# Performance work log

Hardware: AMD Instinct MI355X
Metric: run time of the kernel (lower is better)

The kernel has to match this reference:

```python
import jax, jax.numpy as jnp
import numpy as np

N, IN, C, H, NC, E, G = 4096, 16, 128, 2, 4, 131072, 64
EPS = 1e-5


def setup_inputs() -> dict:
    key = jax.random.key(0)
    ks = jax.random.split(key, 12)
    def rn(k, shape, scale=0.05):
        return jax.random.normal(k, shape, dtype=jnp.float32) * scale
    return dict(
        x=rn(ks[0], (N, IN), 1.0),
        edge_index=jax.random.randint(ks[1], (2, E), 0, N, dtype=jnp.int32),
        batch=jnp.sort(jax.random.randint(ks[2], (N,), 0, G, dtype=jnp.int32)),
        proj_W=rn(ks[3], (IN, C)), proj_b=jnp.zeros((C,), jnp.float32),
        gcn_W=rn(ks[4], (2, C, C)), gcn_b=jnp.zeros((2, C), jnp.float32),
        attn_qkv_w=rn(ks[5], (2, 3 * C, C)), attn_qkv_b=jnp.zeros((2, 3 * C), jnp.float32),
        attn_out_w=rn(ks[6], (2, C, C)), attn_out_b=jnp.zeros((2, C), jnp.float32),
        bn_gamma=jnp.ones((2, 3, C), jnp.float32), bn_beta=jnp.zeros((2, 3, C), jnp.float32),
        mlp_W1=rn(ks[7], (2, C, 2 * C)), mlp_b1=jnp.zeros((2, 2 * C), jnp.float32),
        mlp_W2=rn(ks[8], (2, 2 * C, C)), mlp_b2=jnp.zeros((2, C), jnp.float32),
        lin_W=rn(ks[9], (C, NC)), lin_b=jnp.zeros((NC,), jnp.float32),
    )


def _bn(h, g, b):
    # PyG BatchNorm (training-mode stats over the node dim, biased var)
    mu = jnp.mean(h, axis=0)
    var = jnp.mean((h - mu) ** 2, axis=0)
    return (h - mu) * jax.lax.rsqrt(var + EPS) * g + b


def _gcn(h_in, W, b, src, dst):
    # GCNConv: x' = D^-1/2 (A+I) D^-1/2 (x W) + b
    h = h_in @ W
    deg = jnp.zeros((N,), h.dtype).at[dst].add(1.0) + 1.0  # +1 self loop
    dinv = jax.lax.rsqrt(deg)
    coef = dinv[src] * dinv[dst]                           # [E]
    out = jax.ops.segment_sum(h[src] * coef[:, None], dst, num_segments=N)
    out = out + h * (dinv * dinv)[:, None]                 # self-loop term
    return out + b


def _mha(x, wqkv, bqkv, wout, bout):
    # batch=None in the source => attention over all N nodes as one sequence
    qkv = x @ wqkv.T + bqkv                                # [N,3C]
    q, k, v = jnp.split(qkv, 3, axis=-1)
    dh = C // H
    q = q.reshape(N, H, dh) * (dh ** -0.5)
    k = k.reshape(N, H, dh)
    v = v.reshape(N, H, dh)
    a = jax.nn.softmax(jnp.einsum('nhd,mhd->hnm', q, k), axis=-1)  # [H,N,N]
    o = jnp.einsum('hnm,mhd->nhd', a, v).reshape(N, C)
    return o @ wout.T + bout


def _forward(x, proj_W, proj_b, gcn_W, gcn_b, attn_qkv_w, attn_qkv_b,
             attn_out_w, attn_out_b, bn_gamma, bn_beta, mlp_W1, mlp_b1,
             mlp_W2, mlp_b2, lin_W, lin_b, edge_index, batch):
    src, dst = edge_index[0], edge_index[1]
    h = x @ proj_W + proj_b
    for l in range(2):  # two structurally-distinct GPS layers
        hl = _bn(_gcn(h, gcn_W[l], gcn_b[l], src, dst) + h, bn_gamma[l, 0], bn_beta[l, 0])
        ha = _bn(_mha(h, attn_qkv_w[l], attn_qkv_b[l], attn_out_w[l], attn_out_b[l]) + h,
                 bn_gamma[l, 1], bn_beta[l, 1])
        o = hl + ha
        m = jax.nn.relu(o @ mlp_W1[l] + mlp_b1[l]) @ mlp_W2[l] + mlp_b2[l]
        h = _bn(o + m, bn_gamma[l, 2], bn_beta[l, 2])
        if l == 0:
            h = jax.nn.relu(h)
    ssum = jax.ops.segment_sum(h, batch, num_segments=G)
    cnt = jax.ops.segment_sum(jnp.ones((N,), h.dtype), batch, num_segments=G)
    pooled = ssum / jnp.maximum(cnt, 1.0)[:, None]
    return pooled @ lin_W + lin_b


def reference(x, edge_index, batch, proj_W, proj_b, gcn_W, gcn_b,
              attn_qkv_w, attn_qkv_b, attn_out_w, attn_out_b,
              bn_gamma, bn_beta, mlp_W1, mlp_b1, mlp_W2, mlp_b2,
              lin_W, lin_b):
    return _forward(x, proj_W, proj_b, gcn_W, gcn_b, attn_qkv_w, attn_qkv_b,
                    attn_out_w, attn_out_b, bn_gamma, bn_beta, mlp_W1, mlp_b1,
                    mlp_W2, mlp_b2, lin_W, lin_b, edge_index, batch)
```

## Files before the change

### kernel.cpp

```cpp
#include <hip/hip_runtime.h>
#include <hip/hip_bf16.h>


constexpr int N_  = 4096;
constexpr int IN_ = 16;
constexpr int C_  = 128;
constexpr int E_  = 131072;
constexpr int G_  = 64;
constexpr float EPSV = 1e-5f;
constexpr int SP_ = 8;

typedef unsigned short u16;
typedef unsigned int u32;
typedef __attribute__((ext_vector_type(8))) short bf16x8;
typedef __attribute__((ext_vector_type(4))) short bf16x4;
typedef __attribute__((ext_vector_type(8))) unsigned short u16x8;
typedef __attribute__((ext_vector_type(4))) float f32x4;

__device__ inline u16 f2bf(float f) {
  union { __hip_bfloat16 b; u16 u; } v;
  v.b = __float2bfloat16(f);
  return v.u;
}
__device__ inline float bf2f(u16 s) {
  union { unsigned u; float f; } v; v.u = ((unsigned)s) << 16;
  return v.f;
}

__global__ __launch_bounds__(256) void prol_k(const float* __restrict__ x,
                                              const float* __restrict__ projW,
                                              const float* __restrict__ projB,
                                              float* __restrict__ h,
                                              const float* __restrict__ gcnW,
                                              const float* __restrict__ qkvW,
                                              const float* __restrict__ outW,
                                              const float* __restrict__ w1,
                                              const float* __restrict__ w2,
                                              u16* __restrict__ Wh,
                                              u16* __restrict__ Wl,
                                              const int* __restrict__ ei,
                                              int* __restrict__ cnt) {
  const int bx = blockIdx.x;
  const int tid = threadIdx.x;
  if (bx < 2048) {
    int idx = bx * 256 + tid;
    int n = idx >> 7, c = idx & 127;
    float acc = projB[c];
#pragma unroll
    for (int k = 0; k < IN_; ++k) acc = fmaf(x[n * IN_ + k], projW[k * C_ + c], acc);
    h[idx] = acc;
    return;
  }
  if (bx >= 2336) {
    int e = (bx - 2336) * 256 + tid;
    atomicAdd(&cnt[ei[E_ + e]], 1);
    return;
  }
  int wb = bx - 2048;
  int l = wb / 144, b = wb % 144;
  const float* src; int dstOff, K, M, trans;
  if (b < 16)       { src = gcnW + l * 16384; dstOff = 0;      K = 128; M = 128; trans = 0; }
  else if (b < 64)  { src = qkvW + l * 49152; dstOff = 16384;  K = 128; M = 0;   trans = 1; b -= 16; }
  else if (b < 80)  { src = outW + l * 16384; dstOff = 65536;  K = 128; M = 0;   trans = 1; b -= 64; }
  else if (b < 112) { src = w1 + l * 32768;   dstOff = 81920;  K = 128; M = 256; trans = 0; b -= 80; }
  else              { src = w2 + l * 32768;   dstOff = 114688; K = 256; M = 128; trans = 0; b -= 112; }
  dstOff += l * 147456;
  int d = b * 1024 + tid * 4;
  float v[4];
  if (trans) {
    const float4 f = *(const float4*)&src[d];
    v[0] = f.x; v[1] = f.y; v[2] = f.z; v[3] = f.w;
  } else {
    int ks = (K == 256) ? 8 : 7;
    int n = d >> ks, k = d & (K - 1);
#pragma unroll
    for (int j = 0; j < 4; ++j) v[j] = src[(size_t)(k + j) * M + n];
  }
  ushort4 hv, lv;
  u16* hp = (u16*)&hv; u16* lp = (u16*)&lv;
#pragma unroll
  for (int j = 0; j < 4; ++j) {
    u16 hh = f2bf(v[j]); hp[j] = hh; lp[j] = f2bf(v[j] - bf2f(hh));
  }
  *(ushort4*)&Wh[dstOff + d] = hv;
  *(ushort4*)&Wl[dstOff + d] = lv;
}

__global__ __launch_bounds__(256) void scan_k(const int* __restrict__ cnt,
                                              int* __restrict__ rowptr,
                                              int* __restrict__ cursor,
                                              float* __restrict__ dinv) {
  __shared__ int part[256];
  const int t = threadIdx.x;
  int v[16], s = 0;
#pragma unroll
  for (int i = 0; i < 16; ++i) { v[i] = cnt[t * 16 + i]; s += v[i]; }
  part[t] = s;
  __syncthreads();
  if (t == 0) {
    int run = 0;
    for (int i = 0; i < 256; ++i) { int x = part[i]; part[i] = run; run += x; }
  }
  __syncthreads();
  int off = part[t];
#pragma unroll
  for (int i = 0; i < 16; ++i) {
    int n = t * 16 + i;
    rowptr[n] = off; cursor[n] = off;
    dinv[n] = rsqrtf((float)v[i] + 1.0f);
    off += v[i];
  }
  if (t == 0) rowptr[N_] = E_;
}

__global__ __launch_bounds__(256) void mgemm_dual_k(const float* __restrict__ A,
                                                    const u16* __restrict__ Bh,
                                                    const u16* __restrict__ Bl,
                                                    const float* __restrict__ qkvB,
                                                    float* __restrict__ t0,
                                                    u16* __restrict__ Qg,
                                                    u16* __restrict__ Kg,
                                                    u16* __restrict__ Vtg,
                                                    const int* __restrict__ ei,
                                                    int* __restrict__ cursor,
                                                    int* __restrict__ csr) {
  constexpr int LD = 72, K = 128;
  __shared__ u16 Ah[64 * LD], Al[64 * LD], Bsh[64 * LD], Bsl[64 * LD];
  const int bx = blockIdx.x;
  const int tid = threadIdx.x;
  if (bx >= 512) {
    int e = (bx - 512) * 256 + tid;
    int d = ei[E_ + e];
    int slot = atomicAdd(&cursor[d], 1);
    csr[slot] = ei[e];
    return;
  }
  const int row0 = (bx >> 3) * 64, col0 = (bx & 7) * 64;
  const int wv = tid >> 6, ln = tid & 63, quad = ln >> 4, c = ln & 15;
  f32x4 acc[4];
#pragma unroll
  for (int i = 0; i < 4; ++i) acc[i] = (f32x4){0.f, 0.f, 0.f, 0.f};

  for (int kt = 0; kt < K; kt += 64) {
    __syncthreads();
#pragma unroll
    for (int i = 0; i < 2; ++i) {
      int ch = tid + i * 256, r = ch >> 3, part = ch & 7;
      const float4 f0 = *(const float4*)&A[(size_t)(row0 + r) * K + kt + part * 8];
      const float4 f1 = *(const float4*)&A[(size_t)(row0 + r) * K + kt + part * 8 + 4];
      float fv[8] = {f0.x, f0.y, f0.z, f0.w, f1.x, f1.y, f1.z, f1.w};
      __attribute__((aligned(16))) u16 hb[8], lb[8];
#pragma unroll
      for (int j = 0; j < 8; ++j) {
        u16 hh = f2bf(fv[j]); hb[j] = hh; lb[j] = f2bf(fv[j] - bf2f(hh));
      }
      *(u16x8*)&Ah[r * LD + part * 8] = *(u16x8*)hb;
      *(u16x8*)&Al[r * LD + part * 8] = *(u16x8*)lb;
      size_t bo = (size_t)(col0 + r) * K + kt + part * 8;
      *(u16x8*)&Bsh[r * LD + part * 8] = *(const u16x8*)&Bh[bo];
      *(u16x8*)&Bsl[r * LD + part * 8] = *(const u16x8*)&Bl[bo];
    }
    __syncthreads();
#pragma unroll
    for (int kq = 0; kq < 2; ++kq) {
      bf16x8 ah = *(const bf16x8*)&Ah[(wv * 16 + c) * LD + kq * 32 + quad * 8];
      bf16x8 al = *(const bf16x8*)&Al[(wv * 16 + c) * LD + kq * 32 + quad * 8];
#pragma unroll
      for (int cb = 0; cb < 4; ++cb) {
        bf16x8 bh = *(const bf16x8*)&Bsh[(cb * 16 + c) * LD + kq * 32 + quad * 8];
        bf16x8 bl = *(const bf16x8*)&Bsl[(cb * 16 + c) * LD + kq * 32 + quad * 8];
        acc[cb] = __builtin_amdgcn_mfma_f32_16x16x32_bf16(al, bh, acc[cb], 0, 0, 0);
        acc[cb] = __builtin_amdgcn_mfma_f32_16x16x32_bf16(ah, bl, acc[cb], 0, 0, 0);
        acc[cb] = __builtin_amdgcn_mfma_f32_16x16x32_bf16(ah, bh, acc[cb], 0, 0, 0);
      }
    }
  }

  const int cls = bx & 7;
  if (cls < 2) {
#pragma unroll
    for (int cb = 0; cb < 4; ++cb)
#pragma unroll
      for (int r = 0; r < 4; ++r) {
        int rr = row0 + wv * 16 + quad * 4 + r;
        t0[(size_t)rr * 128 + col0 + cb * 16 + c] = acc[cb][r];
      }
  } else if (cls < 6) {
    const int isQ = cls < 4, hd = cls & 1;
    const float sc = isQ ? 0.125f : 1.0f;
    u16* dst = isQ ? Qg : Kg;
#pragma unroll
    for (int cb = 0; cb < 4; ++cb) {
      int d = cb * 16 + c;
      float qb = qkvB[col0 - 128 + d];
#pragma unroll
      for (int r = 0; r < 4; ++r) {
        int rr = row0 + wv * 16 + quad * 4 + r;
        dst[((size_t)(hd * N_ + rr)) * 64 + d] = f2bf((acc[cb][r] + qb) * sc);
      }
    }
  } else {
    const int hd = cls & 1;
    u16* vtile = Ah;
    __syncthreads();
#pragma unroll
    for (int cb = 0; cb < 4; ++cb) {
      int d = cb * 16 + c;
      float vb = qkvB[col0 - 128 + d];
#pragma unroll
      for (int r = 0; r < 4; ++r)
        vtile[(wv * 16 + quad * 4 + r) * LD + d] = f2bf(acc[cb][r] + vb);
    }
    __syncthreads();
    int d = tid >> 2, j = tid & 3;
    __attribute__((aligned(16))) u16 buf[16];
#pragma unroll
    for (int m = 0; m < 16; ++m) buf[m] = vtile[(j * 16 + m) * LD + d];
    size_t o = ((size_t)(hd * 64 + d)) * N_ + row0 + j * 16;
    *(u16x8*)&Vtg[o]     = *(u16x8*)&buf[0];
    *(u16x8*)&Vtg[o + 8] = *(u16x8*)&buf[8];
  }
}

__global__ __launch_bounds__(256) void mgemm_k(const float* __restrict__ A,
                                               const u16* __restrict__ Bh,
                                               const u16* __restrict__ Bl,
                                               const float* __restrict__ bias,
                                               float* __restrict__ Cout,
                                               int K, int Ncols, int relu,
                                               const float* __restrict__ resid,
                                               float* __restrict__ sums) {
  constexpr int LD = 72;
  __shared__ u16 Ah[64 * LD], Al[64 * LD], Bsh[64 * LD], Bsl[64 * LD];
  const int tid = threadIdx.x;
  const int row0 = blockIdx.y * 64, col0 = blockIdx.x * 64;
  const int wv = tid >> 6, ln = tid & 63, quad = ln >> 4, c = ln & 15;
  f32x4 acc[4];
#pragma unroll
  for (int i = 0; i < 4; ++i) acc[i] = (f32x4){0.f, 0.f, 0.f, 0.f};

  for (int kt = 0; kt < K; kt += 64) {
    __syncthreads();
#pragma unroll
    for (int i = 0; i < 2; ++i) {
      int ch = tid + i * 256, r = ch >> 3, part = ch & 7;
      const float4 f0 = *(const float4*)&A[(size_t)(row0 + r) * K + kt + part * 8];
      const float4 f1 = *(const float4*)&A[(size_t)(row0 + r) * K + kt + part * 8 + 4];
      float fv[8] = {f0.x, f0.y, f0.z, f0.w, f1.x, f1.y, f1.z, f1.w};
      __attribute__((aligned(16))) u16 hb[8], lb[8];
#pragma unroll
      for (int j = 0; j < 8; ++j) {
        u16 hh = f2bf(fv[j]); hb[j] = hh; lb[j] = f2bf(fv[j] - bf2f(hh));
      }
      *(u16x8*)&Ah[r * LD + part * 8] = *(u16x8*)hb;
      *(u16x8*)&Al[r * LD + part * 8] = *(u16x8*)lb;
      size_t bo = (size_t)(col0 + r) * K + kt + part * 8;
      *(u16x8*)&Bsh[r * LD + part * 8] = *(const u16x8*)&Bh[bo];
      *(u16x8*)&Bsl[r * LD + part * 8] = *(const u16x8*)&Bl[bo];
    }
    __syncthreads();
#pragma unroll
    for (int kq = 0; kq < 2; ++kq) {
      bf16x8 ah = *(const bf16x8*)&Ah[(wv * 16 + c) * LD + kq * 32 + quad * 8];
      bf16x8 al = *(const bf16x8*)&Al[(wv * 16 + c) * LD + kq * 32 + quad * 8];
#pragma unroll
      for (int cb = 0; cb < 4; ++cb) {
        bf16x8 bh = *(const bf16x8*)&Bsh[(cb * 16 + c) * LD + kq * 32 + quad * 8];
        bf16x8 bl = *(const bf16x8*)&Bsl[(cb * 16 + c) * LD + kq * 32 + quad * 8];
        acc[cb] = __builtin_amdgcn_mfma_f32_16x16x32_bf16(al, bh, acc[cb], 0, 0, 0);
        acc[cb] = __builtin_amdgcn_mfma_f32_16x16x32_bf16(ah, bl, acc[cb], 0, 0, 0);
        acc[cb] = __builtin_amdgcn_mfma_f32_16x16x32_bf16(ah, bh, acc[cb], 0, 0, 0);
      }
    }
  }
#pragma unroll
  for (int cb = 0; cb < 4; ++cb) {
    float s = 0.0f, s2 = 0.0f;
#pragma unroll
    for (int r = 0; r < 4; ++r) {
      int rr = row0 + wv * 16 + quad * 4 + r;
      int cc = col0 + cb * 16 + c;
      float o = acc[cb][r] + (bias ? bias[cc] : 0.0f);
      if (resid) o += resid[(size_t)rr * Ncols + cc];
      if (relu) o = fmaxf(o, 0.0f);
      Cout[(size_t)rr * Ncols + cc] = o;
      s += o; s2 = fmaf(o, o, s2);
    }
    if (sums) {
      s  += __shfl_xor(s, 16);  s  += __shfl_xor(s, 32);
      s2 += __shfl_xor(s2, 16); s2 += __shfl_xor(s2, 32);
      if (quad == 0) {
        int cc = col0 + cb * 16 + c;
        atomicAdd(&sums[cc], s);
        atomicAdd(&sums[C_ + cc], s2);
      }
    }
  }
}

__global__ __launch_bounds__(256) void mgemm_attn_k(const float* __restrict__ attnP,
                                                    const float* __restrict__ accLp,
                                                    const u16* __restrict__ Bh,
                                                    const u16* __restrict__ Bl,
                                                    const float* __restrict__ bias,
                                                    float* __restrict__ Cout,
                                                    const float* __restrict__ resid,
                                                    float* __restrict__ sums) {
  constexpr int LD = 72, K = 128;
  __shared__ u16 Ah[64 * LD], Al[64 * LD], Bsh[64 * LD], Bsl[64 * LD];
  const int tid = threadIdx.x;
  const int row0 = blockIdx.y * 64, col0 = blockIdx.x * 64;
  const int wv = tid >> 6, ln = tid & 63, quad = ln >> 4, c = ln & 15;
  f32x4 acc[4];
#pragma unroll
  for (int i = 0; i < 4; ++i) acc[i] = (f32x4){0.f, 0.f, 0.f, 0.f};

  for (int kt = 0; kt < K; kt += 64) {
    const int head = kt >> 6;
    __syncthreads();
#pragma unroll
    for (int i = 0; i < 2; ++i) {
      int ch = tid + i * 256, r = ch >> 3, part = ch & 7;
      float lsum = 0.0f;
#pragma unroll
      for (int sp = 0; sp < SP_; ++sp) lsum += accLp[(sp * 2 + head) * N_ + row0 + r];
      float invl = 1.0f / lsum;
      float fv[8] = {0.f, 0.f, 0.f, 0.f, 0.f, 0.f, 0.f, 0.f};
#pragma unroll
      for (int sp = 0; sp < SP_; ++sp) {
        const float* p = &attnP[((size_t)sp * N_ + row0 + r) * C_ + kt + part * 8];
        const float4 f0 = *(const float4*)p;
        const float4 f1 = *(const float4*)(p + 4);
        fv[0] += f0.x; fv[1] += f0.y; fv[2] += f0.z; fv[3] += f0.w;
        fv[4] += f1.x; fv[5] += f1.y; fv[6] += f1.z; fv[7] += f1.w;
      }
      __attribute__((aligned(16))) u16 hb[8], lb[8];
#pragma unroll
      for (int j = 0; j < 8; ++j) {
        float f = fv[j] * invl;
        u16 hh = f2bf(f); hb[j] = hh; lb[j] = f2bf(f - bf2f(hh));
      }
      *(u16x8*)&Ah[r * LD + part * 8] = *(u16x8*)hb;
      *(u16x8*)&Al[r * LD + part * 8] = *(u16x8*)lb;
      size_t bo = (size_t)(col0 + r) * K + kt + part * 8;
      *(u16x8*)&Bsh[r * LD + part * 8] = *(const u16x8*)&Bh[bo];
      *(u16x8*)&Bsl[r * LD + part * 8] = *(const u16x8*)&Bl[bo];
    }
    __syncthreads();
#pragma unroll
    for (int kq = 0; kq < 2; ++kq) {
      bf16x8 ah = *(const bf16x8*)&Ah[(wv * 16 + c) * LD + kq * 32 + quad * 8];
      bf16x8 al = *(const bf16x8*)&Al[(wv * 16 + c) * LD + kq * 32 + quad * 8];
#pragma unroll
      for (int cb = 0; cb < 4; ++cb) {
        bf16x8 bh = *(const bf16x8*)&Bsh[(cb * 16 + c) * LD + kq * 32 + quad * 8];
        bf16x8 bl = *(const bf16x8*)&Bsl[(cb * 16 + c) * LD + kq * 32 + quad * 8];
        acc[cb] = __builtin_amdgcn_mfma_f32_16x16x32_bf16(al, bh, acc[cb], 0, 0, 0);
        acc[cb] = __builtin_amdgcn_mfma_f32_16x16x32_bf16(ah, bl, acc[cb], 0, 0, 0);
        acc[cb] = __builtin_amdgcn_mfma_f32_16x16x32_bf16(ah, bh, acc[cb], 0, 0, 0);
      }
    }
  }
#pragma unroll
  for (int cb = 0; cb < 4; ++cb) {
    float s = 0.0f, s2 = 0.0f;
#pragma unroll
    for (int r = 0; r < 4; ++r) {
      int rr = row0 + wv * 16 + quad * 4 + r;
      int cc = col0 + cb * 16 + c;
      float o = acc[cb][r] + bias[cc] + resid[(size_t)rr * 128 + cc];
      Cout[(size_t)rr * 128 + cc] = o;
      s += o; s2 = fmaf(o, o, s2);
    }
    s  += __shfl_xor(s, 16);  s  += __shfl_xor(s, 32);
    s2 += __shfl_xor(s2, 16); s2 += __shfl_xor(s2, 32);
    if (quad == 0) {
      int cc = col0 + cb * 16 + c;
      atomicAdd(&sums[cc], s);
      atomicAdd(&sums[C_ + cc], s2);
    }
  }
}

__global__ __launch_bounds__(256) void branch_k(const u16* __restrict__ Qg,
                                                const u16* __restrict__ Kg,
                                                const u16* __restrict__ Vtg,
                                                float* __restrict__ attnP,
                                                float* __restrict__ accLp,
                                                const int* __restrict__ rowptr,
                                                const int* __restrict__ csr,
                                                const float* __restrict__ hw,
                                                const float* __restrict__ dinv,
                                                const float* __restrict__ gbias,
                                                const float* __restrict__ hres,
                                                float* __restrict__ t1,
                                                float* __restrict__ sums0) {
  constexpr int LD = 72;
  __shared__ __attribute__((aligned(16))) u16 smem[2 * 64 * LD];
  const int tid = threadIdx.x;
  const int bx = blockIdx.x;

  if (bx >= 1024) {
    const int b = bx - 1024;
    const int wq = tid >> 6, lane = tid & 63;
    const int n = b * 4 + wq;
    float* ls  = (float*)smem;
    float* ls2 = ls + 512;
    const float din = dinv[n];
    float a0 = fmaf(hw[(size_t)n * C_ + lane], din * din,
                    gbias[lane] + hres[(size_t)n * C_ + lane]);
    float a1 = fmaf(hw[(size_t)n * C_ + lane + 64], din * din,
                    gbias[lane + 64] + hres[(size_t)n * C_ + lane + 64]);
    const int e1 = rowptr[n + 1];
    int e = rowptr[n];
    for (; e + 4 <= e1; e += 4) {
      int s0 = csr[e], s1 = csr[e + 1], s2i = csr[e + 2], s3 = csr[e + 3];
      float w0 = dinv[s0] * din, w1 = dinv[s1] * din;
      float w2 = dinv[s2i] * din, w3 = dinv[s3] * din;
      float x00 = hw[(size_t)s0 * C_ + lane],  x01 = hw[(size_t)s0 * C_ + lane + 64];
      float x10 = hw[(size_t)s1 * C_ + lane],  x11 = hw[(size_t)s1 * C_ + lane + 64];
      float x20 = hw[(size_t)s2i * C_ + lane], x21 = hw[(size_t)s2i * C_ + lane + 64];
      float x30 = hw[(size_t)s3 * C_ + lane],  x31 = hw[(size_t)s3 * C_ + lane + 64];
      a0 = fmaf(x00, w0, a0); a1 = fmaf(x01, w0, a1);
      a0 = fmaf(x10, w1, a0); a1 = fmaf(x11, w1, a1);
      a0 = fmaf(x20, w2, a0); a1 = fmaf(x21, w2, a1);
      a0 = fmaf(x30, w3, a0); a1 = fmaf(x31, w3, a1);
    }
    for (; e < e1; ++e) {
      int si = csr[e];
      float w = dinv[si] * din;
      a0 = fmaf(hw[(size_t)si * C_ + lane], w, a0);
      a1 = fmaf(hw[(size_t)si * C_ + lane + 64], w, a1);
    }
    t1[(size_t)n * C_ + lane]      = a0;
    t1[(size_t)n * C_ + lane + 64] = a1;
    ls[wq * 128 + lane]       = a0;  ls[wq * 128 + lane + 64]  = a1;
    ls2[wq * 128 + lane]      = a0 * a0;
    ls2[wq * 128 + lane + 64] = a1 * a1;
    __syncthreads();
    if (tid < 128) {
      float s  = ls[tid]  + ls[tid + 128]  + ls[tid + 256]  + ls[tid + 384];
      float s2 = ls2[tid] + ls2[tid + 128] + ls2[tid + 256] + ls2[tid + 384];
      atomicAdd(&sums0[tid], s);
      atomicAdd(&sums0[C_ + tid], s2);
    }
    return;
  }

  u16* Ks  = smem;
  u16* Vts = smem + 64 * LD;
  const int fb = bx;
  const int head = fb >> 9, sp = (fb >> 6) & 7, q0 = (fb & 63) * 64;
  const int wv = tid >> 6, ln = tid & 63, quad = ln >> 4, c = ln & 15;
  const int KPS = N_ / SP_;

  bf16x8 qf[2];
#pragma unroll
  for (int kq = 0; kq < 2; ++kq)
    qf[kq] = *(const bf16x8*)&Qg[((size_t)(head * N_ + q0 + wv * 16 + c)) * 64 + kq * 32 + quad * 8];

  f32x4 O[4];
#pragma unroll
  for (int i = 0; i < 4; ++i) O[i] = (f32x4){0.f, 0.f, 0.f, 0.f};
  float lsum = 0.0f;

  for (int it = 0; it < KPS / 64; ++it) {
    const int k0 = sp * KPS + it * 64;
    __syncthreads();
#pragma unroll
    for (int i = 0; i < 2; ++i) {
      int ch = tid + i * 256, row = ch >> 3, part = ch & 7;
      *(u16x8*)&Ks[row * LD + part * 8] =
          *(const u16x8*)&Kg[((size_t)(head * N_ + k0 + row)) * 64 + part * 8];
      *(u16x8*)&Vts[row * LD + part * 8] =
          *(const u16x8*)&Vtg[((size_t)(head * 64 + row)) * N_ + k0 + part * 8];
    }
    __syncthreads();

    bf16x4 pf[4];
#pragma unroll
    for (int kb = 0; kb < 4; ++kb) {
      f32x4 st = (f32x4){0.f, 0.f, 0.f, 0.f};
#pragma unroll
      for (int kq = 0; kq < 2; ++kq) {
        bf16x8 a = *(const bf16x8*)&Ks[(kb * 16 + c) * LD + kq * 32 + quad * 8];
        st = __builtin_amdgcn_mfma_f32_16x16x32_bf16(a, qf[kq], st, 0, 0, 0);
      }
      u16 p0 = f2bf(__expf(st[0] - 8.0f));
      u16 p1 = f2bf(__expf(st[1] - 8.0f));
      u16 p2 = f2bf(__expf(st[2] - 8.0f));
      u16 p3 = f2bf(__expf(st[3] - 8.0f));
      lsum += bf2f(p0) + bf2f(p1) + bf2f(p2) + bf2f(p3);
      pf[kb] = (bf16x4){(short)p0, (short)p1, (short)p2, (short)p3};
    }

#pragma unroll
    for (int db = 0; db < 4; ++db) {
#pragma unroll
      for (int kb = 0; kb < 4; ++kb) {
        bf16x4 va = *(const bf16x4*)&Vts[(db * 16 + c) * LD + kb * 16 + quad * 4];
        O[db] = __builtin_amdgcn_mfma_f32_16x16x16bf16_1k(va, pf[kb], O[db], 0, 0, 0);
      }
    }
  }

  lsum += __shfl_xor(lsum, 16);
  lsum += __shfl_xor(lsum, 32);
  if (ln < 16)
    accLp[(sp * 2 + head) * N_ + q0 + wv * 16 + c] = lsum;

  constexpr int LDO = 68;
  __syncthreads();
  float* OT = (float*)smem;
#pragma unroll
  for (int db = 0; db < 4; ++db)
#pragma unroll
    for (int r = 0; r < 4; ++r)
      OT[(wv * 16 + c) * LDO + db * 16 + quad * 4 + r] = O[db][r];
  __syncthreads();
  {
    const int q_loc = tid >> 2, dblk = tid & 3;
    const float4* srcv = (const float4*)&OT[q_loc * LDO + dblk * 16];
    float4* dstv = (float4*)&attnP[((size_t)sp * N_ + q0 + q_loc) * C_ + head * 64 + dblk * 16];
#pragma unroll
    for (int j = 0; j < 4; ++j) dstv[j] = srcv[j];
  }
}

__global__ __launch_bounds__(256) void bn_finapply2_k(const float* __restrict__ t0,
                                                      const float* __restrict__ t1,
                                                      const float* __restrict__ sums1,
                                                      const float* __restrict__ sums0,
                                                      const float* __restrict__ g1,
                                                      const float* __restrict__ b1v,
                                                      const float* __restrict__ g0,
                                                      const float* __restrict__ b0v,
                                                      float* __restrict__ ob) {
  __shared__ float scl1[128], shf1[128], scl0[128], shf0[128];
  const int t = threadIdx.x;
  if (t < 128) {
    float mu = sums1[t] * (1.0f / N_);
    float var = sums1[C_ + t] * (1.0f / N_) - mu * mu;
    float sc = rsqrtf(var + EPSV) * g1[t];
    scl1[t] = sc; shf1[t] = fmaf(-mu, sc, b1v[t]);
    mu = sums0[t] * (1.0f / N_);
    var = sums0[C_ + t] * (1.0f / N_) - mu * mu;
    sc = rsqrtf(var + EPSV) * g0[t];
    scl0[t] = sc; shf0[t] = fmaf(-mu, sc, b0v[t]);
  }
  __syncthreads();
  int idx = blockIdx.x * 256 + t;
  int c = idx & 127;
  ob[idx] = fmaf(t0[idx], scl1[c], shf1[c]) + fmaf(t1[idx], scl0[c], shf0[c]);
}

__global__ __launch_bounds__(256) void bn_finapply_k(const float* __restrict__ A,
                                                     const float* __restrict__ sums,
                                                     const float* __restrict__ g,
                                                     const float* __restrict__ b,
                                                     float* __restrict__ outp, int relu,
                                                     const int* __restrict__ batch,
                                                     float* __restrict__ pooled) {
  __shared__ float s_scl[128], s_shf[128];
  const int t = threadIdx.x;
  if (t < 128) {
    float mu = sums[t] * (1.0f / N_);
    float var = sums[C_ + t] * (1.0f / N_) - mu * mu;
    float sc = rsqrtf(var + EPSV) * g[t];
    s_scl[t] = sc;
    s_shf[t] = fmaf(-mu, sc, b[t]);
  }
  __syncthreads();
  int idx = blockIdx.x * 256 + t;
  int c = idx & 127;
  float v = fmaf(A[idx], s_scl[c], s_shf[c]);
  if (relu) v = fmaxf(v, 0.0f);
  outp[idx] = v;
  if (pooled) {
    int n = idx >> 7;
    atomicAdd(&pooled[(size_t)batch[n] * C_ + c], v);
  }
}

__global__ __launch_bounds__(256) void final_k(const float* __restrict__ pooled,
                                               const int* __restrict__ batch,
                                               const float* __restrict__ W,
                                               const float* __restrict__ b,
                                               float* __restrict__ out) {
  int t = threadIdx.x;
  int g = t >> 2, j = t & 3;
  int lo = 0, hi = N_;
  while (lo < hi) { int m = (lo + hi) >> 1; if (batch[m] < g) lo = m + 1; else hi = m; }
  int st = lo; lo = 0; hi = N_;
  while (lo < hi) { int m = (lo + hi) >> 1; if (batch[m] < g + 1) lo = m + 1; else hi = m; }
  float inv = 1.0f / fmaxf((float)(lo - st), 1.0f);
  float acc = b[j];
  for (int c = 0; c < C_; ++c) acc = fmaf(pooled[(size_t)g * C_ + c] * inv, W[c * 4 + j], acc);
  out[t] = acc;
}

extern "C" void kernel_launch(void* const* d_in, const int* in_sizes, int n_in,
                              void* d_out, int out_size, void* d_ws, size_t ws_size,
                              hipStream_t stream) {
  const float* x     = (const float*)d_in[0];
  const int*   ei    = (const int*)d_in[1];
  const int*   batch = (const int*)d_in[2];
  const float* projW = (const float*)d_in[3];
  const float* projB = (const float*)d_in[4];
  const float* gcnW  = (const float*)d_in[5];
  const float* gcnB  = (const float*)d_in[6];
  const float* qkvW  = (const float*)d_in[7];
  const float* qkvB  = (const float*)d_in[8];
  const float* outW  = (const float*)d_in[9];
  const float* outB  = (const float*)d_in[10];
  const float* bnG   = (const float*)d_in[11];
  const float* bnB   = (const float*)d_in[12];
  const float* w1    = (const float*)d_in[13];
  const float* b1    = (const float*)d_in[14];
  const float* w2    = (const float*)d_in[15];
  const float* b2    = (const float*)d_in[16];
  const float* linW  = (const float*)d_in[17];
  const float* linB  = (const float*)d_in[18];
  float* out = (float*)d_out;

  const size_t NC = (size_t)N_ * C_;
  const size_t HB = (size_t)2 * N_ * 64;
  float* ws   = (float*)d_ws;
  float* h    = ws;
  float* t0   = ws + 1 * NC;
  float* t1   = ws + 2 * NC;
  float* ob   = ws + 3 * NC;
  u16* Qg  = (u16*)(ws + 4 * NC);
  u16* Kg  = Qg + HB;
  u16* Vtg = Kg + HB;
  float* attnP = ws + 6 * NC;
  float* m1b   = attnP;
  float* accLp = ws + (6 + SP_) * NC;
  float* sums  = accLp + 2 * SP_ * N_;
  float* pooled = sums + 6 * 256;
  int*   icnt = (int*)(pooled + (size_t)G_ * C_);
  float* dinv = (float*)(icnt + N_);
  int*   rowptr = (int*)(dinv + N_);
  int*   cursor = rowptr + N_ + 1;
  int*   csr    = cursor + N_;
  u16*   Wh = (u16*)(csr + E_);
  u16*   Wl = Wh + 2 * 147456;

  const dim3 b256(256);

  hipMemsetAsync(sums, 0, (6 * 256 + (size_t)G_ * C_ + N_) * sizeof(float), stream);

  prol_k<<<2848, b256, 0, stream>>>(x, projW, projB, h, gcnW, qkvW, outW,
                                    w1, w2, Wh, Wl, ei, icnt);
  scan_k<<<1, b256, 0, stream>>>(icnt, rowptr, cursor, dinv);

  for (int l = 0; l < 2; ++l) {
    const size_t WL = (size_t)l * 147456;
    float* sums0 = sums + (l * 3 + 0) * 256;
    float* sums1 = sums + (l * 3 + 1) * 256;
    float* sums2 = sums + (l * 3 + 2) * 256;

    mgemm_dual_k<<<(l == 0) ? 1024 : 512, b256, 0, stream>>>(
        h, Wh + WL, Wl + WL, qkvB + l * 384, t0, Qg, Kg, Vtg, ei, cursor, csr);
    branch_k<<<2048, b256, 0, stream>>>(Qg, Kg, Vtg, attnP, accLp,
                                        rowptr, csr, t0, dinv, gcnB + l * C_,
                                        h, t1, sums0);
    mgemm_attn_k<<<dim3(2, 64), b256, 0, stream>>>(attnP, accLp,
                                                   Wh + WL + 65536, Wl + WL + 65536,
                                                   outB + l * C_, t0, h, sums1);
    bn_finapply2_k<<<(int)(NC / 256), b256, 0, stream>>>(
        t0, t1, sums1, sums0,
        bnG + (l * 3 + 1) * C_, bnB + (l * 3 + 1) * C_,
        bnG + (l * 3 + 0) * C_, bnB + (l * 3 + 0) * C_, ob);
    mgemm_k<<<dim3(4, 64), b256, 0, stream>>>(ob, Wh + WL + 81920, Wl + WL + 81920,
                                              b1 + l * 256, m1b, 128, 256, 1,
                                              nullptr, nullptr);
    mgemm_k<<<dim3(2, 64), b256, 0, stream>>>(m1b, Wh + WL + 114688, Wl + WL + 114688,
                                              b2 + l * C_, t0, 256, 128, 0,
                                              ob, sums2);
    bn_finapply_k<<<(int)(NC / 256), b256, 0, stream>>>(
        t0, sums2, bnG + (l * 3 + 2) * C_, bnB + (l * 3 + 2) * C_, h,
        (l == 0) ? 1 : 0, batch, (l == 1) ? pooled : nullptr);
  }

  final_k<<<1, 256, 0, stream>>>(pooled, batch, linW, linB, out);
}
```

Measured before the change: 328.4 us.

## Process two query tiles per wave in attention to reuse K/V LDS loads

Each attention block now covers 128 queries instead of 64: every wave computes two 16-query sub-tiles that share each K and V fragment read from LDS, which halves the number of attention blocks from 1024 to 512. The goal is to halve the global-to-LDS K/V traffic per query and the LDS reads per MFMA. The output epilogue is staged through shared memory in two halves, and the grid shrinks accordingly. In exchange, register use per wave roughly doubles and there are fewer blocks, which can lower occupancy.

Result: faster. 316.2 us (-3.7%).

```diff
diff --git a/kernel.cpp b/kernel.cpp
--- a/kernel.cpp
+++ b/kernel.cpp
@@ -400,8 +400,8 @@
   const int tid = threadIdx.x;
   const int bx = blockIdx.x;
 
-  if (bx >= 1024) {
-    const int b = bx - 1024;
+  if (bx >= 512) {
+    const int b = bx - 512;
     const int wq = tid >> 6, lane = tid & 63;
     const int n = b * 4 + wq;
     float* ls  = (float*)smem;
@@ -450,19 +450,25 @@
   u16* Ks  = smem;
   u16* Vts = smem + 64 * LD;
   const int fb = bx;
-  const int head = fb >> 9, sp = (fb >> 6) & 7, q0 = (fb & 63) * 64;
+  const int head = fb >> 8, sp = (fb >> 5) & 7, q0 = (fb & 31) * 128;
   const int wv = tid >> 6, ln = tid & 63, quad = ln >> 4, c = ln & 15;
   const int KPS = N_ / SP_;
-
-  bf16x8 qf[2];
-#pragma unroll
-  for (int kq = 0; kq < 2; ++kq)
-    qf[kq] = *(const bf16x8*)&Qg[((size_t)(head * N_ + q0 + wv * 16 + c)) * 64 + kq * 32 + quad * 8];
-
-  f32x4 O[4];
-#pragma unroll
-  for (int i = 0; i < 4; ++i) O[i] = (f32x4){0.f, 0.f, 0.f, 0.f};
-  float lsum = 0.0f;
+  const int qb = q0 + wv * 32;
+
+  bf16x8 qfA[2], qfB[2];
+#pragma unroll
+  for (int kq = 0; kq < 2; ++kq) {
+    qfA[kq] = *(const bf16x8*)&Qg[((size_t)(head * N_ + qb + c)) * 64 + kq * 32 + quad * 8];
+    qfB[kq] = *(const bf16x8*)&Qg[((size_t)(head * N_ + qb + 16 + c)) * 64 + kq * 32 + quad * 8];
+  }
+
+  f32x4 OA[4], OB[4];
+#pragma unroll
+  for (int i = 0; i < 4; ++i) {
+    OA[i] = (f32x4){0.f, 0.f, 0.f, 0.f};
+    OB[i] = (f32x4){0.f, 0.f, 0.f, 0.f};
+  }
+  float lsumA = 0.0f, lsumB = 0.0f;
 
   for (int it = 0; it < KPS / 64; ++it) {
     const int k0 = sp * KPS + it * 64;
@@ -477,21 +483,29 @@
     }
     __syncthreads();
 
-    bf16x4 pf[4];
+    bf16x4 pfA[4], pfB[4];
 #pragma unroll
     for (int kb = 0; kb < 4; ++kb) {
-      f32x4 st = (f32x4){0.f, 0.f, 0.f, 0.f};
+      f32x4 stA = (f32x4){0.f, 0.f, 0.f, 0.f};
+      f32x4 stB = (f32x4){0.f, 0.f, 0.f, 0.f};
 #pragma unroll
       for (int kq = 0; kq < 2; ++kq) {
         bf16x8 a = *(const bf16x8*)&Ks[(kb * 16 + c) * LD + kq * 32 + quad * 8];
-        st = __builtin_amdgcn_mfma_f32_16x16x32_bf16(a, qf[kq], st, 0, 0, 0);
-      }
-      u16 p0 = f2bf(__expf(st[0] - 8.0f));
-      u16 p1 = f2bf(__expf(st[1] - 8.0f));
-      u16 p2 = f2bf(__expf(st[2] - 8.0f));
-      u16 p3 = f2bf(__expf(st[3] - 8.0f));
-      lsum += bf2f(p0) + bf2f(p1) + bf2f(p2) + bf2f(p3);
-      pf[kb] = (bf16x4){(short)p0, (short)p1, (short)p2, (short)p3};
+        stA = __builtin_amdgcn_mfma_f32_16x16x32_bf16(a, qfA[kq], stA, 0, 0, 0);
+        stB = __builtin_amdgcn_mfma_f32_16x16x32_bf16(a, qfB[kq], stB, 0, 0, 0);
+      }
+      u16 a0 = f2bf(__expf(stA[0] - 8.0f));
+      u16 a1 = f2bf(__expf(stA[1] - 8.0f));
+      u16 a2 = f2bf(__expf(stA[2] - 8.0f));
+      u16 a3 = f2bf(__expf(stA[3] - 8.0f));
+      lsumA += bf2f(a0) + bf2f(a1) + bf2f(a2) + bf2f(a3);
+      pfA[kb] = (bf16x4){(short)a0, (short)a1, (short)a2, (short)a3};
+      u16 b0 = f2bf(__expf(stB[0] - 8.0f));
+      u16 b1 = f2bf(__expf(stB[1] - 8.0f));
+      u16 b2 = f2bf(__expf(stB[2] - 8.0f));
+      u16 b3 = f2bf(__expf(stB[3] - 8.0f));
+      lsumB += bf2f(b0) + bf2f(b1) + bf2f(b2) + bf2f(b3);
+      pfB[kb] = (bf16x4){(short)b0, (short)b1, (short)b2, (short)b3};
     }
 
 #pragma unroll
@@ -499,31 +513,43 @@
 #pragma unroll
       for (int kb = 0; kb < 4; ++kb) {
         bf16x4 va = *(const bf16x4*)&Vts[(db * 16 + c) * LD + kb * 16 + quad * 4];
-        O[db] = __builtin_amdgcn_mfma_f32_16x16x16bf16_1k(va, pf[kb], O[db], 0, 0, 0);
-      }
-    }
-  }
-
-  lsum += __shfl_xor(lsum, 16);
-  lsum += __shfl_xor(lsum, 32);
-  if (ln < 16)
-    accLp[(sp * 2 + head) * N_ + q0 + wv * 16 + c] = lsum;
+        OA[db] = __builtin_amdgcn_mfma_f32_16x16x16bf16_1k(va, pfA[kb], OA[db], 0, 0, 0);
+        OB[db] = __builtin_amdgcn_mfma_f32_16x16x16bf16_1k(va, pfB[kb], OB[db], 0, 0, 0);
+      }
+    }
+  }
+
+  lsumA += __shfl_xor(lsumA, 16); lsumA += __shfl_xor(lsumA, 32);
+  lsumB += __shfl_xor(lsumB, 16); lsumB += __shfl_xor(lsumB, 32);
+  if (ln < 16) {
+    accLp[(sp * 2 + head) * N_ + qb + c]      = lsumA;
+    accLp[(sp * 2 + head) * N_ + qb + 16 + c] = lsumB;
+  }
 
   constexpr int LDO = 68;
+  float* OT = (float*)smem;
   __syncthreads();
-  float* OT = (float*)smem;
-#pragma unroll
-  for (int db = 0; db < 4; ++db)
-#pragma unroll
-    for (int r = 0; r < 4; ++r)
-      OT[(wv * 16 + c) * LDO + db * 16 + quad * 4 + r] = O[db][r];
-  __syncthreads();
-  {
-    const int q_loc = tid >> 2, dblk = tid & 3;
-    const float4* srcv = (const float4*)&OT[q_loc * LDO + dblk * 16];
-    float4* dstv = (float4*)&attnP[((size_t)sp * N_ + q0 + q_loc) * C_ + head * 64 + dblk * 16];
-#pragma unroll
-    for (int j = 0; j < 4; ++j) dstv[j] = srcv[j];
+#pragma unroll
+  for (int hh = 0; hh < 2; ++hh) {
+    if ((wv >> 1) == hh) {
+      const int lq = (wv & 1) * 32;
+#pragma unroll
+      for (int db = 0; db < 4; ++db)
+#pragma unroll
+        for (int r = 0; r < 4; ++r) {
+          OT[(lq + c) * LDO + db * 16 + quad * 4 + r]      = OA[db][r];
+          OT[(lq + 16 + c) * LDO + db * 16 + quad * 4 + r] = OB[db][r];
+        }
+    }
+    __syncthreads();
+    {
+      const int q_loc = tid >> 2, dblk = tid & 3;
+      const float4* srcv = (const float4*)&OT[q_loc * LDO + dblk * 16];
+      float4* dstv = (float4*)&attnP[((size_t)sp * N_ + q0 + hh * 64 + q_loc) * C_ + head * 64 + dblk * 16];
+#pragma unroll
+      for (int j = 0; j < 4; ++j) dstv[j] = srcv[j];
+    }
+    if (hh == 0) __syncthreads();
   }
 }
 
@@ -662,7 +688,7 @@
 
     mgemm_dual_k<<<(l == 0) ? 1024 : 512, b256, 0, stream>>>(
         h, Wh + WL, Wl + WL, qkvB + l * 384, t0, Qg, Kg, Vtg, ei, cursor, csr);
-    branch_k<<<2048, b256, 0, stream>>>(Qg, Kg, Vtg, attnP, accLp,
+    branch_k<<<1536, b256, 0, stream>>>(Qg, Kg, Vtg, attnP, accLp,
                                         rowptr, csr, t0, dinv, gcnB + l * C_,
                                         h, t1, sums0);
     mgemm_attn_k<<<dim3(2, 64), b256, 0, stream>>>(attnP, accLp,
```
